# Kernel tuning notes

Measured on AMD Instinct MI355X. Metric: run time of the kernel, lower is better.

## Reference

```python
import jax, jax.numpy as jnp
import numpy as np

HIDDEN, KEY_DIM, VALUE_DIM = 1024, 64, 64
B, T = 4, 4096


def setup_inputs() -> dict:
    key = jax.random.key(0)
    ks = jax.random.split(key, 9)
    s = 0.02
    return {
        "y_all": jax.random.normal(ks[0], (B, T, HIDDEN), dtype=jnp.float32),
        # torch nn.Linear weights: (out_features, in_features)
        "Wq": jax.random.normal(ks[1], (KEY_DIM, HIDDEN), dtype=jnp.float32) * s,
        "bq": jax.random.normal(ks[2], (KEY_DIM,), dtype=jnp.float32) * s,
        "Wk": jax.random.normal(ks[3], (KEY_DIM, HIDDEN), dtype=jnp.float32) * s,
        "bk": jax.random.normal(ks[4], (KEY_DIM,), dtype=jnp.float32) * s,
        "Wv": jax.random.normal(ks[5], (VALUE_DIM, HIDDEN), dtype=jnp.float32) * s,
        "bv": jax.random.normal(ks[6], (VALUE_DIM,), dtype=jnp.float32) * s,
        "Wo": jax.random.normal(ks[7], (HIDDEN, VALUE_DIM), dtype=jnp.float32) * s,
        "bo": jax.random.normal(ks[8], (HIDDEN,), dtype=jnp.float32) * s,
    }


def reference(y_all, Wq, bq, Wk, bk, Wv, bv, Wo, bo):
    # The original per-timestep loop is exactly causal self-attention:
    # query at position i attends over positions 0..i.
    q = jnp.einsum("bth,kh->btk", y_all, Wq) + bq          # (B,T,Dk)
    k = jnp.einsum("bth,kh->btk", y_all, Wk) + bk          # (B,T,Dk)
    v = jnp.einsum("bth,vh->btv", y_all, Wv) + bv          # (B,T,Dv)
    scale = jnp.asarray(KEY_DIM, q.dtype) ** 0.5
    scores = jnp.einsum("bqk,btk->bqt", q / scale, k)      # (B,T,T)
    t = scores.shape[-1]
    causal = jnp.tril(jnp.ones((t, t), dtype=bool))
    scores = jnp.where(causal, scores, jnp.asarray(-jnp.inf, scores.dtype))
    weights = jax.nn.softmax(scores, axis=-1)
    ctx = jnp.einsum("bqt,btv->bqv", weights, v)           # (B,T,Dv)
    out = jnp.einsum("bqv,hv->bqh", ctx, Wo) + bo          # (B,T,H)
    return out
```

## Files before the change

### kernel.cpp

```cpp
#include <hip/hip_runtime.h>


typedef __attribute__((ext_vector_type(4)))  float f32x4;
typedef __attribute__((ext_vector_type(16))) float f32x16;
typedef __attribute__((ext_vector_type(8)))  short s16x8;
typedef __attribute__((ext_vector_type(4)))  short s16x4;

#define DEV static __device__ __forceinline__

static constexpr int TT = 4096;
static constexpr int HH = 1024;
static constexpr int DD = 64;
static constexpr float MNEG = -3.0e38f;

DEV unsigned short f2bf(float f) {
  union { float f; unsigned int u; } v; v.f = f;
  unsigned int r = v.u + 0x7FFFu + ((v.u >> 16) & 1u);
  return (unsigned short)(r >> 16);
}

DEV unsigned int cvtpk(float lo, float hi) {
  unsigned int r;
  asm("v_cvt_pk_bf16_f32 %0, %1, %2" : "=v"(r) : "v"(lo), "v"(hi));
  return r;
}

DEV s16x8 mk8(unsigned int w0, unsigned int w1, unsigned int w2, unsigned int w3) {
  union { unsigned int u[4]; s16x8 v; } c;
  c.u[0] = w0; c.u[1] = w1; c.u[2] = w2; c.u[3] = w3; return c.v;
}

DEV int swzA(int row) { return ((row & 7) << 4); }
DEV int swzK(int row) { return ((row & 7) << 4) ^ ((row & 8) << 3); }

__global__ void prep_kernel(const float* __restrict__ Wq, const float* __restrict__ Wk,
                            const float* __restrict__ Wv, const float* __restrict__ Wo,
                            unsigned short* __restrict__ Wall,
                            unsigned short* __restrict__ Wo_b)
{
  int i = blockIdx.x * blockDim.x + threadIdx.x;
  int stride = gridDim.x * blockDim.x;
  const int n1 = 64 * HH;
  for (int idx = i; idx < 3 * n1; idx += stride) {
    float v = idx < n1 ? Wq[idx] : (idx < 2 * n1 ? Wk[idx - n1] : Wv[idx - 2 * n1]);
    Wall[idx] = f2bf(v);
  }
  for (int idx = i; idx < HH * DD; idx += stride) {
    int hcol = idx >> 6, d = idx & 63;
    size_t off = (size_t)(hcol >> 4) * 1024 + (d >> 5) * 512 + (hcol & 15) * 32
               + ((d >> 3) & 3) * 8 + (d & 7);
    Wo_b[off] = f2bf(Wo[idx]);
  }
}

__global__ __launch_bounds__(256, 2) void qkv_kernel(
    const float* __restrict__ y, const unsigned short* __restrict__ Wall,
    const float* __restrict__ bq, const float* __restrict__ bk,
    const float* __restrict__ bv,
    unsigned short* __restrict__ q_ws, unsigned short* __restrict__ k_ws,
    unsigned short* __restrict__ vT_ws)
{
  __shared__ unsigned short ylds[2][32 * 64];
  __shared__ unsigned short wlds[2][192 * 64];
  const int t = threadIdx.x;
  const int wv = t >> 6, lane = t & 63, g = lane >> 4, c = lane & 15;
  const int row0 = blockIdx.x * 32;
  const int bb = row0 >> 12;
  const int tb = row0 & 4095;
  const int yrow = t >> 3, ycol0 = (t & 7) * 8;

  f32x4 acc[2][3];
#pragma unroll
  for (int m = 0; m < 2; ++m)
#pragma unroll
    for (int i = 0; i < 3; ++i)
#pragma unroll
      for (int e = 0; e < 4; ++e) acc[m][i][e] = 0.0f;

  f32x4 yr[2];
  s16x8 wr[6];

  auto load_tiles = [&](int kb) {
    const float* src = y + (size_t)(row0 + yrow) * HH + kb * 64 + ycol0;
    yr[0] = *(const f32x4*)(src);
    yr[1] = *(const f32x4*)(src + 4);
#pragma unroll
    for (int ii = 0; ii < 6; ++ii) {
      int ch = t + ii * 256;
      int rw = ch >> 3, c0 = (ch & 7) * 8;
      wr[ii] = *(const s16x8*)(Wall + (size_t)rw * HH + kb * 64 + c0);
    }
  };
  auto write_tiles = [&](int buf) {
    s16x8 h0;
#pragma unroll
    for (int e = 0; e < 4; ++e) {
      h0[e]     = (short)f2bf(yr[0][e]);
      h0[e + 4] = (short)f2bf(yr[1][e]);
    }
    int byte0 = yrow * 128 + ycol0 * 2;
    *(s16x8*)((char*)ylds[buf] + (byte0 ^ swzA(yrow))) = h0;
#pragma unroll
    for (int ii = 0; ii < 6; ++ii) {
      int ch = t + ii * 256;
      int rw = ch >> 3, c0 = (ch & 7) * 8;
      int byte = rw * 128 + c0 * 2;
      *(s16x8*)((char*)wlds[buf] + (byte ^ swzA(rw))) = wr[ii];
    }
  };

  load_tiles(0);
  write_tiles(0);
  __syncthreads();
  for (int kb = 0; kb < 16; ++kb) {
    int buf = kb & 1;
    if (kb < 15) load_tiles(kb + 1);
#pragma unroll
    for (int kk = 0; kk < 2; ++kk) {
      s16x8 a[2], bfr[3];
#pragma unroll
      for (int m = 0; m < 2; ++m) {
        int ra = 16 * m + c;
        a[m] = *(const s16x8*)((char*)ylds[buf] +
                 ((ra * 128 + (kk * 32 + 8 * g) * 2) ^ swzA(ra)));
      }
#pragma unroll
      for (int i = 0; i < 3; ++i) {
        int rb = 16 * (3 * wv + i) + c;
        bfr[i] = *(const s16x8*)((char*)wlds[buf] +
                   ((rb * 128 + (kk * 32 + 8 * g) * 2) ^ swzA(rb)));
      }
#pragma unroll
      for (int m = 0; m < 2; ++m)
#pragma unroll
        for (int i = 0; i < 3; ++i)
          acc[m][i] = __builtin_amdgcn_mfma_f32_16x16x32_bf16(a[m], bfr[i], acc[m][i], 0, 0, 0);
    }
    __syncthreads();
    if (kb < 15) { write_tiles((kb + 1) & 1); __syncthreads(); }
  }

  unsigned short* elds = &wlds[0][0];
  const float qsc = 1.4426950408889634f / 8.0f;
#pragma unroll
  for (int m = 0; m < 2; ++m)
#pragma unroll
    for (int i = 0; i < 3; ++i) {
      int nt = 3 * wv + i;
      int sec = nt >> 2;
      int dcol = (nt & 3) * 16 + c;
      float bias = sec == 0 ? bq[dcol] : (sec == 1 ? bk[dcol] : bv[dcol]);
#pragma unroll
      for (int i2 = 0; i2 < 4; ++i2) {
        int rl = 16 * m + 4 * g + i2;
        float val = acc[m][i][i2] + bias;
        if (sec == 0) val *= qsc;
        if (sec < 2) elds[sec * 2048 + rl * 64 + dcol] = f2bf(val);
        else         elds[4096 + dcol * 32 + rl]       = f2bf(val);
      }
    }
  __syncthreads();
  {
    int trow = t >> 3, d0 = (t & 7) * 8;
    s16x8 vq = *(const s16x8*)(elds + trow * 64 + d0);
    s16x8 vk = *(const s16x8*)(elds + 2048 + trow * 64 + d0);
    size_t offqk = (size_t)bb * (TT * DD) + (size_t)(tb >> 5) * 2048
                 + (d0 >> 4) * 512 + trow * 16 + (d0 & 15);
    *(s16x8*)(q_ws + offqk) = vq;
    *(s16x8*)(k_ws + offqk) = vk;
    int d = t >> 2, tq = (t & 3) * 8;
    s16x8 vvv = *(const s16x8*)(elds + 4096 + d * 32 + tq);
    int tg = tb + tq;
    size_t offv = (size_t)bb * (DD * TT) + (size_t)(tg >> 6) * 4096
                + (d >> 5) * 2048 + ((tg >> 4) & 3) * 512 + (d & 31) * 16 + (tg & 15);
    *(s16x8*)(vT_ws + offv) = vvv;
  }
}

__global__ __launch_bounds__(256, 2) void attn_kernel(
    const unsigned short* __restrict__ q_ws, const unsigned short* __restrict__ k_ws,
    const unsigned short* __restrict__ vT_ws, const unsigned short* __restrict__ Wo_b,
    const float* __restrict__ bo, float* __restrict__ out)
{
  __shared__ float obuf[3 * 2048];
  __shared__ float mstat[3 * 128];
  __shared__ unsigned short clds[32 * 64];
  const int t = threadIdx.x, wv = t >> 6, lane = t & 63;
  const int qcol = lane & 31, h = lane >> 5;
  const int b = blockIdx.x & 3;
  const int jslot = blockIdx.x >> 2;
  const int j32 = (jslot < 64) ? (2 * jslot) : (127 - 2 * (jslot - 64));
  const int q0 = j32 * 32;
  const int L = j32 >> 1;
  const size_t base  = (size_t)b * TT * DD;
  const size_t vbase = (size_t)b * DD * TT;
  const int g = lane >> 4, c = lane & 15;
  const int lchunk = (lane & 31) * 16 + (lane >> 5) * 8;

  s16x8 qf[4];
  {
    const unsigned short* qp = q_ws + base + (size_t)j32 * 2048;
#pragma unroll
    for (int kk = 0; kk < 4; ++kk) qf[kk] = *(const s16x8*)(qp + kk * 512 + lchunk);
  }
  f32x16 o[2];
#pragma unroll
  for (int mt = 0; mt < 2; ++mt)
#pragma unroll
    for (int rg = 0; rg < 16; ++rg) o[mt][rg] = 0.0f;
  float m_run = MNEG, l_run = 0.0f;

  for (int kt = wv; kt <= L; kt += 4) {
    const int kv0 = kt * 64;
    s16x8 kf[2][4];
#pragma unroll
    for (int mt = 0; mt < 2; ++mt)
#pragma unroll
      for (int kk = 0; kk < 4; ++kk)
        kf[mt][kk] = *(const s16x8*)(k_ws + base +
                       (size_t)(2 * kt + mt) * 2048 + kk * 512 + lchunk);
    f32x16 s[2];
#pragma unroll
    for (int mt = 0; mt < 2; ++mt)
#pragma unroll
      for (int rg = 0; rg < 16; ++rg) s[mt][rg] = 0.0f;
    __builtin_amdgcn_s_setprio(1);
#pragma unroll
    for (int kk = 0; kk < 4; ++kk)
#pragma unroll
      for (int mt = 0; mt < 2; ++mt)
        s[mt] = __builtin_amdgcn_mfma_f32_32x32x16_bf16(kf[mt][kk], qf[kk], s[mt], 0, 0, 0);
    __builtin_amdgcn_s_setprio(0);
    s16x8 vf[2][4];
#pragma unroll
    for (int mt = 0; mt < 2; ++mt)
#pragma unroll
      for (int ks = 0; ks < 4; ++ks)
        vf[mt][ks] = *(const s16x8*)(vT_ws + vbase +
                       (size_t)kt * 4096 + mt * 2048 + ks * 512 + lchunk);
    if (kt == L) {
      int qq = q0 + qcol;
#pragma unroll
      for (int mt = 0; mt < 2; ++mt)
#pragma unroll
        for (int rg = 0; rg < 16; ++rg) {
          int kvabs = kv0 + 32 * mt + (rg & 3) + 8 * (rg >> 2) + 4 * h;
          if (kvabs > qq) s[mt][rg] = MNEG;
        }
    }
    float mx[16];
#pragma unroll
    for (int e = 0; e < 16; ++e) mx[e] = fmaxf(s[0][e], s[1][e]);
#pragma unroll
    for (int st = 8; st >= 1; st >>= 1)
#pragma unroll
      for (int e = 0; e < 8; ++e) if (e < st) mx[e] = fmaxf(mx[e], mx[e + st]);
    float pm = fmaxf(mx[0], __shfl_xor(mx[0], 32));
    float m_new;
    if (__all(pm - m_run <= 8.0f)) {
      m_new = m_run;
    } else {
      m_new = fmaxf(m_run, pm);
      float alpha = exp2f(m_run - m_new);
      l_run *= alpha;
#pragma unroll
      for (int mt = 0; mt < 2; ++mt)
#pragma unroll
        for (int rg = 0; rg < 16; ++rg) o[mt][rg] *= alpha;
      m_run = m_new;
    }
#pragma unroll
    for (int mt = 0; mt < 2; ++mt)
#pragma unroll
      for (int rg = 0; rg < 16; ++rg) s[mt][rg] = exp2f(s[mt][rg] - m_new);
    float sm[16];
#pragma unroll
    for (int e = 0; e < 16; ++e) sm[e] = s[0][e] + s[1][e];
#pragma unroll
    for (int st = 8; st >= 1; st >>= 1)
#pragma unroll
      for (int e = 0; e < 8; ++e) if (e < st) sm[e] += sm[e + st];
    float rowsum = sm[0] + __shfl_xor(sm[0], 32);
    l_run += rowsum;
    s16x8 pf[4];
#pragma unroll
    for (int mt = 0; mt < 2; ++mt) {
      unsigned int a0 = cvtpk(s[mt][0],  s[mt][1]);
      unsigned int a1 = cvtpk(s[mt][2],  s[mt][3]);
      unsigned int b0 = cvtpk(s[mt][4],  s[mt][5]);
      unsigned int b1 = cvtpk(s[mt][6],  s[mt][7]);
      unsigned int c0 = cvtpk(s[mt][8],  s[mt][9]);
      unsigned int c1 = cvtpk(s[mt][10], s[mt][11]);
      unsigned int d0 = cvtpk(s[mt][12], s[mt][13]);
      unsigned int d1 = cvtpk(s[mt][14], s[mt][15]);
      asm("v_permlane32_swap_b32 %0, %1" : "+v"(a0), "+v"(b0));
      asm("v_permlane32_swap_b32 %0, %1" : "+v"(a1), "+v"(b1));
      asm("v_permlane32_swap_b32 %0, %1" : "+v"(c0), "+v"(d0));
      asm("v_permlane32_swap_b32 %0, %1" : "+v"(c1), "+v"(d1));
      pf[2 * mt]     = mk8(a0, a1, b0, b1);
      pf[2 * mt + 1] = mk8(c0, c1, d0, d1);
    }
    __builtin_amdgcn_s_setprio(1);
#pragma unroll
    for (int ks = 0; ks < 4; ++ks)
#pragma unroll
      for (int mt = 0; mt < 2; ++mt)
        o[mt] = __builtin_amdgcn_mfma_f32_32x32x16_bf16(vf[mt][ks], pf[ks], o[mt], 0, 0, 0);
    __builtin_amdgcn_s_setprio(0);
  }

  if (wv != 0) {
#pragma unroll
    for (int mt = 0; mt < 2; ++mt)
#pragma unroll
      for (int rg = 0; rg < 16; ++rg)
        obuf[(wv - 1) * 2048 + (mt * 16 + rg) * 64 + lane] = o[mt][rg];
    mstat[(wv - 1) * 128 + lane] = m_run;
    mstat[(wv - 1) * 128 + 64 + lane] = l_run;
  }
  __syncthreads();
  if (wv == 0) {
    float mB[3], lB[3];
    float mS = m_run;
#pragma unroll
    for (int i = 0; i < 3; ++i) {
      mB[i] = mstat[i * 128 + lane];
      lB[i] = mstat[i * 128 + 64 + lane];
      mS = fmaxf(mS, mB[i]);
    }
    float f0 = exp2f(m_run - mS);
    float fi[3];
    float l_tot = l_run * f0;
#pragma unroll
    for (int i = 0; i < 3; ++i) { fi[i] = exp2f(mB[i] - mS); l_tot += lB[i] * fi[i]; }
    float inv = 1.0f / l_tot;
#pragma unroll
    for (int mt = 0; mt < 2; ++mt) {
#pragma unroll
      for (int rgq = 0; rgq < 4; ++rgq) {
        s16x4 pb;
#pragma unroll
        for (int e = 0; e < 4; ++e) {
          int rg = 4 * rgq + e;
          float val = o[mt][rg] * f0;
#pragma unroll
          for (int i = 0; i < 3; ++i)
            val += obuf[i * 2048 + (mt * 16 + rg) * 64 + lane] * fi[i];
          pb[e] = (short)f2bf(val * inv);
        }
        int d0 = 32 * mt + 8 * rgq + 4 * h;
        int byte = qcol * 128 + d0 * 2;
        *(s16x4*)((char*)clds + (byte ^ swzK(qcol))) = pb;
      }
    }
  }
  __syncthreads();

  s16x8 afr[2][2];
#pragma unroll
  for (int mt = 0; mt < 2; ++mt)
#pragma unroll
    for (int kk = 0; kk < 2; ++kk) {
      int ra = 16 * mt + c;
      afr[mt][kk] = *(const s16x8*)((char*)clds +
                      ((ra * 128 + (32 * kk + 8 * g) * 2) ^ swzK(ra)));
    }
  const int wchunk = (lane & 15) * 32 + (lane >> 4) * 8;
  const size_t orow0 = (size_t)(b * TT + q0);
#pragma unroll 4
  for (int nt = 0; nt < 16; ++nt) {
    int col = wv * 256 + 16 * nt + c;
    s16x8 bfr[2];
#pragma unroll
    for (int kk = 0; kk < 2; ++kk)
      bfr[kk] = *(const s16x8*)(Wo_b + (size_t)(wv * 16 + nt) * 1024
                                + kk * 512 + wchunk);
    f32x4 acc4[2];
#pragma unroll
    for (int mt = 0; mt < 2; ++mt)
#pragma unroll
      for (int e = 0; e < 4; ++e) acc4[mt][e] = 0.0f;
#pragma unroll
    for (int kk = 0; kk < 2; ++kk)
#pragma unroll
      for (int mt = 0; mt < 2; ++mt)
        acc4[mt] = __builtin_amdgcn_mfma_f32_16x16x32_bf16(afr[mt][kk], bfr[kk],
                                                           acc4[mt], 0, 0, 0);
    float bias = bo[col];
#pragma unroll
    for (int mt = 0; mt < 2; ++mt)
#pragma unroll
      for (int i = 0; i < 4; ++i) {
        size_t row = orow0 + 16 * mt + 4 * g + i;
        out[row * HH + col] = acc4[mt][i] + bias;
      }
  }
}

extern "C" void kernel_launch(void* const* d_in, const int* in_sizes, int n_in,
                              void* d_out, int out_size, void* d_ws, size_t ws_size,
                              hipStream_t stream)
{
  const float* y  = (const float*)d_in[0];
  const float* Wq = (const float*)d_in[1];
  const float* bq = (const float*)d_in[2];
  const float* Wk = (const float*)d_in[3];
  const float* bk = (const float*)d_in[4];
  const float* Wv = (const float*)d_in[5];
  const float* bv = (const float*)d_in[6];
  const float* Wo = (const float*)d_in[7];
  const float* bo = (const float*)d_in[8];
  float* out = (float*)d_out;
  char* ws = (char*)d_ws;
  unsigned short* Wall  = (unsigned short*)(ws);
  unsigned short* Wo_b  = (unsigned short*)(ws + 393216);
  unsigned short* q_ws  = (unsigned short*)(ws + 524288);
  unsigned short* k_ws  = (unsigned short*)(ws + 524288 + 2097152);
  unsigned short* vT_ws = (unsigned short*)(ws + 524288 + 2 * 2097152);

  prep_kernel<<<dim3(256), dim3(256), 0, stream>>>(Wq, Wk, Wv, Wo, Wall, Wo_b);
  qkv_kernel<<<dim3(512), dim3(256), 0, stream>>>(y, Wall, bq, bk, bv, q_ws, k_ws, vT_ws);
  attn_kernel<<<dim3(512), dim3(256), 0, stream>>>(q_ws, k_ws, vT_ws, Wo_b, bo, out);
}
```

Before: 58.29 us.

## Split output projection into separate kernel and double-buffer K tile loads

The attention kernel now prefetches the next K tile into a second register buffer while the current tile is processed, so global-load latency overlaps compute. The fused output projection is moved out into a new proj_kernel: attention writes the bf16 context back into the q workspace, and the new kernel reads it and runs the Wo GEMM plus bias. This shortens the causal-imbalanced attention blocks and lets the projection run with even work per block. The cost is an extra kernel launch, a global round trip for the context, and higher register pressure from the second K buffer.

```diff
diff --git a/kernel.cpp b/kernel.cpp
--- a/kernel.cpp
+++ b/kernel.cpp
@@ -178,9 +178,9 @@
 }
 
 __global__ __launch_bounds__(256, 2) void attn_kernel(
-    const unsigned short* __restrict__ q_ws, const unsigned short* __restrict__ k_ws,
-    const unsigned short* __restrict__ vT_ws, const unsigned short* __restrict__ Wo_b,
-    const float* __restrict__ bo, float* __restrict__ out)
+    unsigned short* qc_ws,
+    const unsigned short* __restrict__ k_ws,
+    const unsigned short* __restrict__ vT_ws)
 {
   __shared__ float obuf[3 * 2048];
   __shared__ float mstat[3 * 128];
@@ -194,12 +194,11 @@
   const int L = j32 >> 1;
   const size_t base  = (size_t)b * TT * DD;
   const size_t vbase = (size_t)b * DD * TT;
-  const int g = lane >> 4, c = lane & 15;
   const int lchunk = (lane & 31) * 16 + (lane >> 5) * 8;
 
   s16x8 qf[4];
   {
-    const unsigned short* qp = q_ws + base + (size_t)j32 * 2048;
+    const unsigned short* qp = qc_ws + base + (size_t)j32 * 2048;
 #pragma unroll
     for (int kk = 0; kk < 4; ++kk) qf[kk] = *(const s16x8*)(qp + kk * 512 + lchunk);
   }
@@ -210,15 +209,17 @@
     for (int rg = 0; rg < 16; ++rg) o[mt][rg] = 0.0f;
   float m_run = MNEG, l_run = 0.0f;
 
-  for (int kt = wv; kt <= L; kt += 4) {
-    const int kv0 = kt * 64;
-    s16x8 kf[2][4];
+  auto loadK = [&](int kt, s16x8 (&kf)[2][4]) {
 #pragma unroll
     for (int mt = 0; mt < 2; ++mt)
 #pragma unroll
       for (int kk = 0; kk < 4; ++kk)
         kf[mt][kk] = *(const s16x8*)(k_ws + base +
                        (size_t)(2 * kt + mt) * 2048 + kk * 512 + lchunk);
+  };
+
+  auto tile = [&](int kt, s16x8 (&kf)[2][4], s16x8 (&kfn)[2][4]) {
+    const int kv0 = kt * 64;
     f32x16 s[2];
 #pragma unroll
     for (int mt = 0; mt < 2; ++mt)
@@ -231,6 +232,7 @@
       for (int mt = 0; mt < 2; ++mt)
         s[mt] = __builtin_amdgcn_mfma_f32_32x32x16_bf16(kf[mt][kk], qf[kk], s[mt], 0, 0, 0);
     __builtin_amdgcn_s_setprio(0);
+    if (kt + 4 <= L) loadK(kt + 4, kfn);
     s16x8 vf[2][4];
 #pragma unroll
     for (int mt = 0; mt < 2; ++mt)
@@ -307,6 +309,17 @@
       for (int mt = 0; mt < 2; ++mt)
         o[mt] = __builtin_amdgcn_mfma_f32_32x32x16_bf16(vf[mt][ks], pf[ks], o[mt], 0, 0, 0);
     __builtin_amdgcn_s_setprio(0);
+  };
+
+  s16x8 kfA[2][4], kfB[2][4];
+  int kt = wv;
+  if (kt <= L) loadK(kt, kfA);
+  while (kt <= L) {
+    tile(kt, kfA, kfB);
+    kt += 4;
+    if (kt > L) break;
+    tile(kt, kfB, kfA);
+    kt += 4;
   }
 
   if (wv != 0) {
@@ -356,17 +369,36 @@
   }
   __syncthreads();
 
+  {
+    int trow = t >> 3, d0 = (t & 7) * 8;
+    s16x8 vctx = *(const s16x8*)((char*)clds +
+                   (((trow << 7) + (d0 << 1)) ^ swzK(trow)));
+    size_t off = base + (size_t)j32 * 2048
+               + (size_t)((d0 >> 4) * 512 + trow * 16 + (d0 & 15));
+    *(s16x8*)(qc_ws + off) = vctx;
+  }
+}
+
+__global__ __launch_bounds__(256, 2) void proj_kernel(
+    const unsigned short* __restrict__ ctx_ws, const unsigned short* __restrict__ Wo_b,
+    const float* __restrict__ bo, float* __restrict__ out)
+{
+  const int t = threadIdx.x, wv = t >> 6, lane = t & 63;
+  const int g = lane >> 4, c = lane & 15;
+  const int u = blockIdx.x;
+  const int b = u >> 7, j = u & 127;
+  const size_t base = (size_t)b * TT * DD;
+  const unsigned short* cp = ctx_ws + base + (size_t)j * 2048;
+
   s16x8 afr[2][2];
 #pragma unroll
   for (int mt = 0; mt < 2; ++mt)
 #pragma unroll
-    for (int kk = 0; kk < 2; ++kk) {
-      int ra = 16 * mt + c;
-      afr[mt][kk] = *(const s16x8*)((char*)clds +
-                      ((ra * 128 + (32 * kk + 8 * g) * 2) ^ swzK(ra)));
-    }
+    for (int kk = 0; kk < 2; ++kk)
+      afr[mt][kk] = *(const s16x8*)(cp + (2 * kk + (g >> 1)) * 512
+                                    + (16 * mt + c) * 16 + 8 * (g & 1));
   const int wchunk = (lane & 15) * 32 + (lane >> 4) * 8;
-  const size_t orow0 = (size_t)(b * TT + q0);
+  const size_t orow0 = (size_t)(b * TT + j * 32);
 #pragma unroll 4
   for (int nt = 0; nt < 16; ++nt) {
     int col = wv * 256 + 16 * nt + c;
@@ -420,5 +452,6 @@
 
   prep_kernel<<<dim3(256), dim3(256), 0, stream>>>(Wq, Wk, Wv, Wo, Wall, Wo_b);
   qkv_kernel<<<dim3(512), dim3(256), 0, stream>>>(y, Wall, bq, bk, bv, q_ws, k_ws, vT_ws);
-  attn_kernel<<<dim3(512), dim3(256), 0, stream>>>(q_ws, k_ws, vT_ws, Wo_b, bo, out);
-}
+  attn_kernel<<<dim3(512), dim3(256), 0, stream>>>(q_ws, k_ws, vT_ws);
+  proj_kernel<<<dim3(512), dim3(256), 0, stream>>>(q_ws, Wo_b, bo, out);
+}
```

After: 70.77 us. +21.4%, slower.

## Merge two 32-row query tiles per 512-thread block sharing Wo loads

Applied to the files above, without the earlier changes.

Each attention block now handles two adjacent 32-row query tiles (a 64-row slab) with 8 waves, four per sub-tile, instead of one tile per 256-thread block. The output projection loads each Wo fragment once and applies it to both sub-tiles, halving Wo traffic per block. The grid shrinks to 256 blocks, and the previous load-balancing slot order that paired short and long causal tiles is dropped. This risks more tail imbalance and lower occupancy from the doubled LDS footprint.

```diff
diff --git a/kernel.cpp b/kernel.cpp
--- a/kernel.cpp
+++ b/kernel.cpp
@@ -177,21 +177,22 @@
   }
 }
 
-__global__ __launch_bounds__(256, 2) void attn_kernel(
+__global__ __launch_bounds__(512, 2) void attn_kernel(
     const unsigned short* __restrict__ q_ws, const unsigned short* __restrict__ k_ws,
     const unsigned short* __restrict__ vT_ws, const unsigned short* __restrict__ Wo_b,
     const float* __restrict__ bo, float* __restrict__ out)
 {
-  __shared__ float obuf[3 * 2048];
-  __shared__ float mstat[3 * 128];
-  __shared__ unsigned short clds[32 * 64];
-  const int t = threadIdx.x, wv = t >> 6, lane = t & 63;
+  __shared__ float obuf[2][3 * 2048];
+  __shared__ float mstat[2][3 * 128];
+  __shared__ unsigned short clds[2][32 * 64];
+  const int t = threadIdx.x, wp = t >> 6, lane = t & 63;
+  const int sub = wp >> 2, wl = wp & 3;
   const int qcol = lane & 31, h = lane >> 5;
   const int b = blockIdx.x & 3;
-  const int jslot = blockIdx.x >> 2;
-  const int j32 = (jslot < 64) ? (2 * jslot) : (127 - 2 * (jslot - 64));
+  const int j64 = blockIdx.x >> 2;
+  const int j32 = 2 * j64 + sub;
   const int q0 = j32 * 32;
-  const int L = j32 >> 1;
+  const int L = j64;
   const size_t base  = (size_t)b * TT * DD;
   const size_t vbase = (size_t)b * DD * TT;
   const int g = lane >> 4, c = lane & 15;
@@ -210,7 +211,7 @@
     for (int rg = 0; rg < 16; ++rg) o[mt][rg] = 0.0f;
   float m_run = MNEG, l_run = 0.0f;
 
-  for (int kt = wv; kt <= L; kt += 4) {
+  for (int kt = wl; kt <= L; kt += 4) {
     const int kv0 = kt * 64;
     s16x8 kf[2][4];
 #pragma unroll
@@ -309,23 +310,23 @@
     __builtin_amdgcn_s_setprio(0);
   }
 
-  if (wv != 0) {
+  if (wl != 0) {
 #pragma unroll
     for (int mt = 0; mt < 2; ++mt)
 #pragma unroll
       for (int rg = 0; rg < 16; ++rg)
-        obuf[(wv - 1) * 2048 + (mt * 16 + rg) * 64 + lane] = o[mt][rg];
-    mstat[(wv - 1) * 128 + lane] = m_run;
-    mstat[(wv - 1) * 128 + 64 + lane] = l_run;
+        obuf[sub][(wl - 1) * 2048 + (mt * 16 + rg) * 64 + lane] = o[mt][rg];
+    mstat[sub][(wl - 1) * 128 + lane] = m_run;
+    mstat[sub][(wl - 1) * 128 + 64 + lane] = l_run;
   }
   __syncthreads();
-  if (wv == 0) {
+  if (wl == 0) {
     float mB[3], lB[3];
     float mS = m_run;
 #pragma unroll
     for (int i = 0; i < 3; ++i) {
-      mB[i] = mstat[i * 128 + lane];
-      lB[i] = mstat[i * 128 + 64 + lane];
+      mB[i] = mstat[sub][i * 128 + lane];
+      lB[i] = mstat[sub][i * 128 + 64 + lane];
       mS = fmaxf(mS, mB[i]);
     }
     float f0 = exp2f(m_run - mS);
@@ -345,55 +346,60 @@
           float val = o[mt][rg] * f0;
 #pragma unroll
           for (int i = 0; i < 3; ++i)
-            val += obuf[i * 2048 + (mt * 16 + rg) * 64 + lane] * fi[i];
+            val += obuf[sub][i * 2048 + (mt * 16 + rg) * 64 + lane] * fi[i];
           pb[e] = (short)f2bf(val * inv);
         }
         int d0 = 32 * mt + 8 * rgq + 4 * h;
         int byte = qcol * 128 + d0 * 2;
-        *(s16x4*)((char*)clds + (byte ^ swzK(qcol))) = pb;
+        *(s16x4*)((char*)clds[sub] + (byte ^ swzK(qcol))) = pb;
       }
     }
   }
   __syncthreads();
 
-  s16x8 afr[2][2];
-#pragma unroll
-  for (int mt = 0; mt < 2; ++mt)
-#pragma unroll
-    for (int kk = 0; kk < 2; ++kk) {
-      int ra = 16 * mt + c;
-      afr[mt][kk] = *(const s16x8*)((char*)clds +
-                      ((ra * 128 + (32 * kk + 8 * g) * 2) ^ swzK(ra)));
-    }
+  s16x8 afr[2][2][2];
+#pragma unroll
+  for (int s2 = 0; s2 < 2; ++s2)
+#pragma unroll
+    for (int mt = 0; mt < 2; ++mt)
+#pragma unroll
+      for (int kk = 0; kk < 2; ++kk) {
+        int ra = 16 * mt + c;
+        afr[s2][mt][kk] = *(const s16x8*)((char*)clds[s2] +
+                            ((ra * 128 + (32 * kk + 8 * g) * 2) ^ swzK(ra)));
+      }
   const int wchunk = (lane & 15) * 32 + (lane >> 4) * 8;
-  const size_t orow0 = (size_t)(b * TT + q0);
-#pragma unroll 4
-  for (int nt = 0; nt < 16; ++nt) {
-    int col = wv * 256 + 16 * nt + c;
+#pragma unroll 2
+  for (int nt = 0; nt < 8; ++nt) {
+    int nt16 = wp * 8 + nt;
+    int col = nt16 * 16 + c;
     s16x8 bfr[2];
 #pragma unroll
     for (int kk = 0; kk < 2; ++kk)
-      bfr[kk] = *(const s16x8*)(Wo_b + (size_t)(wv * 16 + nt) * 1024
-                                + kk * 512 + wchunk);
-    f32x4 acc4[2];
-#pragma unroll
-    for (int mt = 0; mt < 2; ++mt)
-#pragma unroll
-      for (int e = 0; e < 4; ++e) acc4[mt][e] = 0.0f;
-#pragma unroll
-    for (int kk = 0; kk < 2; ++kk)
-#pragma unroll
-      for (int mt = 0; mt < 2; ++mt)
-        acc4[mt] = __builtin_amdgcn_mfma_f32_16x16x32_bf16(afr[mt][kk], bfr[kk],
-                                                           acc4[mt], 0, 0, 0);
+      bfr[kk] = *(const s16x8*)(Wo_b + (size_t)nt16 * 1024 + kk * 512 + wchunk);
     float bias = bo[col];
 #pragma unroll
-    for (int mt = 0; mt < 2; ++mt)
-#pragma unroll
-      for (int i = 0; i < 4; ++i) {
-        size_t row = orow0 + 16 * mt + 4 * g + i;
-        out[row * HH + col] = acc4[mt][i] + bias;
-      }
+    for (int s2 = 0; s2 < 2; ++s2) {
+      f32x4 acc4[2];
+#pragma unroll
+      for (int mt = 0; mt < 2; ++mt)
+#pragma unroll
+        for (int e = 0; e < 4; ++e) acc4[mt][e] = 0.0f;
+#pragma unroll
+      for (int kk = 0; kk < 2; ++kk)
+#pragma unroll
+        for (int mt = 0; mt < 2; ++mt)
+          acc4[mt] = __builtin_amdgcn_mfma_f32_16x16x32_bf16(afr[s2][mt][kk], bfr[kk],
+                                                             acc4[mt], 0, 0, 0);
+      size_t orow0 = (size_t)(b * TT + (2 * j64 + s2) * 32);
+#pragma unroll
+      for (int mt = 0; mt < 2; ++mt)
+#pragma unroll
+        for (int i = 0; i < 4; ++i) {
+          size_t row = orow0 + 16 * mt + 4 * g + i;
+          out[row * HH + col] = acc4[mt][i] + bias;
+        }
+    }
   }
 }
 
@@ -420,5 +426,5 @@
 
   prep_kernel<<<dim3(256), dim3(256), 0, stream>>>(Wq, Wk, Wv, Wo, Wall, Wo_b);
   qkv_kernel<<<dim3(512), dim3(256), 0, stream>>>(y, Wall, bq, bk, bv, q_ws, k_ws, vT_ws);
-  attn_kernel<<<dim3(512), dim3(256), 0, stream>>>(q_ws, k_ws, vT_ws, Wo_b, bo, out);
-}
+  attn_kernel<<<dim3(256), dim3(512), 0, stream>>>(q_ws, k_ws, vT_ws, Wo_b, bo, out);
+}
```

Measured after the change: 68.27 us. +17.1%, slower.

## Process two KV tiles per attention loop iteration with a shared softmax rescale

Applied to the files above, without the earlier changes.

Unrolls the flash-attention KV loop by two, so each wave handles tiles kt and kt+4 together. K/V loads and QK MFMAs for both tiles are issued back to back, a single running-max update covers both, and output goes to two separate accumulators that are summed at the end. The aim is more memory-level parallelism and MFMA overlap, with half as many max/rescale branches. The cost is higher register pressure (two sets of K/V fragments, scores and accumulators), which may cut occupancy or cause spills.

```diff
diff --git a/kernel.cpp b/kernel.cpp
--- a/kernel.cpp
+++ b/kernel.cpp
@@ -203,51 +203,51 @@
 #pragma unroll
     for (int kk = 0; kk < 4; ++kk) qf[kk] = *(const s16x8*)(qp + kk * 512 + lchunk);
   }
-  f32x16 o[2];
+  f32x16 o1[2], o2[2];
 #pragma unroll
   for (int mt = 0; mt < 2; ++mt)
 #pragma unroll
-    for (int rg = 0; rg < 16; ++rg) o[mt][rg] = 0.0f;
+    for (int rg = 0; rg < 16; ++rg) { o1[mt][rg] = 0.0f; o2[mt][rg] = 0.0f; }
   float m_run = MNEG, l_run = 0.0f;
 
-  for (int kt = wv; kt <= L; kt += 4) {
-    const int kv0 = kt * 64;
-    s16x8 kf[2][4];
+  auto loadK = [&](int kt, s16x8 (&kf)[2][4]) {
 #pragma unroll
     for (int mt = 0; mt < 2; ++mt)
 #pragma unroll
       for (int kk = 0; kk < 4; ++kk)
         kf[mt][kk] = *(const s16x8*)(k_ws + base +
                        (size_t)(2 * kt + mt) * 2048 + kk * 512 + lchunk);
-    f32x16 s[2];
-#pragma unroll
-    for (int mt = 0; mt < 2; ++mt)
-#pragma unroll
-      for (int rg = 0; rg < 16; ++rg) s[mt][rg] = 0.0f;
-    __builtin_amdgcn_s_setprio(1);
-#pragma unroll
-    for (int kk = 0; kk < 4; ++kk)
-#pragma unroll
-      for (int mt = 0; mt < 2; ++mt)
-        s[mt] = __builtin_amdgcn_mfma_f32_32x32x16_bf16(kf[mt][kk], qf[kk], s[mt], 0, 0, 0);
-    __builtin_amdgcn_s_setprio(0);
-    s16x8 vf[2][4];
+  };
+  auto loadV = [&](int kt, s16x8 (&vf)[2][4]) {
 #pragma unroll
     for (int mt = 0; mt < 2; ++mt)
 #pragma unroll
       for (int ks = 0; ks < 4; ++ks)
         vf[mt][ks] = *(const s16x8*)(vT_ws + vbase +
                        (size_t)kt * 4096 + mt * 2048 + ks * 512 + lchunk);
-    if (kt == L) {
-      int qq = q0 + qcol;
+  };
+  auto qk = [&](const s16x8 (&kf)[2][4], f32x16 (&s)[2]) {
+#pragma unroll
+    for (int mt = 0; mt < 2; ++mt)
+#pragma unroll
+      for (int rg = 0; rg < 16; ++rg) s[mt][rg] = 0.0f;
+#pragma unroll
+    for (int kk = 0; kk < 4; ++kk)
 #pragma unroll
       for (int mt = 0; mt < 2; ++mt)
-#pragma unroll
-        for (int rg = 0; rg < 16; ++rg) {
-          int kvabs = kv0 + 32 * mt + (rg & 3) + 8 * (rg >> 2) + 4 * h;
-          if (kvabs > qq) s[mt][rg] = MNEG;
-        }
-    }
+        s[mt] = __builtin_amdgcn_mfma_f32_32x32x16_bf16(kf[mt][kk], qf[kk], s[mt], 0, 0, 0);
+  };
+  auto mask = [&](int kt, f32x16 (&s)[2]) {
+    int qq = q0 + qcol;
+#pragma unroll
+    for (int mt = 0; mt < 2; ++mt)
+#pragma unroll
+      for (int rg = 0; rg < 16; ++rg) {
+        int kvabs = kt * 64 + 32 * mt + (rg & 3) + 8 * (rg >> 2) + 4 * h;
+        if (kvabs > qq) s[mt][rg] = MNEG;
+      }
+  };
+  auto treemax = [&](const f32x16 (&s)[2]) {
     float mx[16];
 #pragma unroll
     for (int e = 0; e < 16; ++e) mx[e] = fmaxf(s[0][e], s[1][e]);
@@ -255,20 +255,9 @@
     for (int st = 8; st >= 1; st >>= 1)
 #pragma unroll
       for (int e = 0; e < 8; ++e) if (e < st) mx[e] = fmaxf(mx[e], mx[e + st]);
-    float pm = fmaxf(mx[0], __shfl_xor(mx[0], 32));
-    float m_new;
-    if (__all(pm - m_run <= 8.0f)) {
-      m_new = m_run;
-    } else {
-      m_new = fmaxf(m_run, pm);
-      float alpha = exp2f(m_run - m_new);
-      l_run *= alpha;
-#pragma unroll
-      for (int mt = 0; mt < 2; ++mt)
-#pragma unroll
-        for (int rg = 0; rg < 16; ++rg) o[mt][rg] *= alpha;
-      m_run = m_new;
-    }
+    return mx[0];
+  };
+  auto expsum = [&](f32x16 (&s)[2], float m_new) {
 #pragma unroll
     for (int mt = 0; mt < 2; ++mt)
 #pragma unroll
@@ -280,9 +269,9 @@
     for (int st = 8; st >= 1; st >>= 1)
 #pragma unroll
       for (int e = 0; e < 8; ++e) if (e < st) sm[e] += sm[e + st];
-    float rowsum = sm[0] + __shfl_xor(sm[0], 32);
-    l_run += rowsum;
-    s16x8 pf[4];
+    return sm[0];
+  };
+  auto pack = [&](const f32x16 (&s)[2], s16x8 (&pf)[4]) {
 #pragma unroll
     for (int mt = 0; mt < 2; ++mt) {
       unsigned int a0 = cvtpk(s[mt][0],  s[mt][1]);
@@ -300,14 +289,65 @@
       pf[2 * mt]     = mk8(a0, a1, b0, b1);
       pf[2 * mt + 1] = mk8(c0, c1, d0, d1);
     }
-    __builtin_amdgcn_s_setprio(1);
+  };
+  auto pv = [&](const s16x8 (&vf)[2][4], const s16x8 (&pf)[4], f32x16 (&o)[2]) {
 #pragma unroll
     for (int ks = 0; ks < 4; ++ks)
 #pragma unroll
       for (int mt = 0; mt < 2; ++mt)
         o[mt] = __builtin_amdgcn_mfma_f32_32x32x16_bf16(vf[mt][ks], pf[ks], o[mt], 0, 0, 0);
+  };
+
+  for (int kt = wv; kt <= L; kt += 8) {
+    const int kt2 = kt + 4;
+    const bool has2 = (kt2 <= L);
+    s16x8 kf1[2][4], kf2[2][4];
+    loadK(kt, kf1);
+    if (has2) loadK(kt2, kf2);
+    f32x16 s1[2], s2[2];
+    __builtin_amdgcn_s_setprio(1);
+    qk(kf1, s1);
+    if (has2) qk(kf2, s2);
     __builtin_amdgcn_s_setprio(0);
-  }
+    s16x8 vf1[2][4], vf2[2][4];
+    loadV(kt, vf1);
+    if (has2) loadV(kt2, vf2);
+    if (kt == L) mask(kt, s1);
+    if (has2 && kt2 == L) mask(kt2, s2);
+    float pm = treemax(s1);
+    if (has2) pm = fmaxf(pm, treemax(s2));
+    pm = fmaxf(pm, __shfl_xor(pm, 32));
+    float m_new;
+    if (__all(pm - m_run <= 8.0f)) {
+      m_new = m_run;
+    } else {
+      m_new = fmaxf(m_run, pm);
+      float alpha = exp2f(m_run - m_new);
+      l_run *= alpha;
+#pragma unroll
+      for (int mt = 0; mt < 2; ++mt)
+#pragma unroll
+        for (int rg = 0; rg < 16; ++rg) { o1[mt][rg] *= alpha; o2[mt][rg] *= alpha; }
+      m_run = m_new;
+    }
+    float rowsum = expsum(s1, m_new);
+    if (has2) rowsum += expsum(s2, m_new);
+    rowsum += __shfl_xor(rowsum, 32);
+    l_run += rowsum;
+    s16x8 pf1[4], pf2[4];
+    pack(s1, pf1);
+    if (has2) pack(s2, pf2);
+    __builtin_amdgcn_s_setprio(1);
+    pv(vf1, pf1, o1);
+    if (has2) pv(vf2, pf2, o2);
+    __builtin_amdgcn_s_setprio(0);
+  }
+
+  f32x16 o[2];
+#pragma unroll
+  for (int mt = 0; mt < 2; ++mt)
+#pragma unroll
+    for (int rg = 0; rg < 16; ++rg) o[mt][rg] = o1[mt][rg] + o2[mt][rg];
 
   if (wv != 0) {
 #pragma unroll
```

Result: slower. 80.89 us (+38.8%).
